# Kernel tuning notes

Hardware: AMD Instinct MI355X
Metric: run time of the kernel (lower is better)

Reference implementation:

```python
import jax, jax.numpy as jnp
import numpy as np


def setup_inputs() -> dict:
    key = jax.random.key(0)
    k1, k2, k3 = jax.random.split(key, 3)
    N, E, D_IN, D_OUT = 100000, 3200000, 256, 256
    x = jax.random.normal(k1, (N, D_IN), dtype=jnp.float32)
    W = jax.random.normal(k2, (D_OUT, D_IN), dtype=jnp.float32) * (1.0 / np.sqrt(D_IN))
    edge_index = jax.random.randint(k3, (2, E), 0, N, dtype=jnp.int32)
    return {"x": x, "W": W, "edge_index": edge_index}


def reference(x, W, edge_index):
    N = x.shape[0]
    # add self loops (static shape: E + N edges)
    loops = jnp.arange(N, dtype=edge_index.dtype)
    src = jnp.concatenate([edge_index[0], loops])  # [E+N]
    dst = jnp.concatenate([edge_index[1], loops])  # [E+N]
    # symmetric degree normalization: deg = bincount over source index
    deg = jax.ops.segment_sum(jnp.ones_like(src, dtype=x.dtype), src, num_segments=N)
    deg_rsqrt = jax.lax.rsqrt(deg)
    vals = deg_rsqrt[src] * deg_rsqrt[dst]  # [E+N]
    # dense projection then SpMM: out[i] = sum_e A[src_e=i] * h[dst_e]
    h = x @ W.T  # [N, D_OUT]
    msgs = vals[:, None] * h[dst]  # gather + scale
    out = jax.ops.segment_sum(msgs, src, num_segments=N)  # scatter-add
    return out
```

## Files before the change

kernel.cpp:

```cpp
#include <hip/hip_runtime.h>
#include <hip/hip_bf16.h>
#include <stdint.h>

#define D 256
#define NBUCK 391
#define BSHIFT 8
#define TILE 4096

typedef short short8 __attribute__((ext_vector_type(8)));
typedef float f32x4 __attribute__((ext_vector_type(4)));

__device__ __forceinline__ float bf2f(unsigned short u) {
  return __uint_as_float(((unsigned)u) << 16);
}
__device__ __forceinline__ unsigned short f2bf(float f) {
  unsigned u = __float_as_uint(f);
  unsigned r = u + 0x7FFFu + ((u >> 16) & 1u);
  return (unsigned short)(r >> 16);
}

__global__ void bucket_hist_kernel(const int* __restrict__ src, int* __restrict__ bcount, int E) {
  __shared__ int h[NBUCK];
  for (int i = threadIdx.x; i < NBUCK; i += 256) h[i] = 0;
  __syncthreads();
  int gid = blockIdx.x * 256 + threadIdx.x;
  for (int e = gid; e < E; e += 256 * 256) atomicAdd(&h[src[e] >> BSHIFT], 1);
  __syncthreads();
  for (int i = threadIdx.x; i < NBUCK; i += 256) {
    int c = h[i];
    if (c) atomicAdd(&bcount[i], c);
  }
}

__global__ void bucket_scan_kernel(const int* __restrict__ bcount, int* __restrict__ bbase,
                                   int* __restrict__ gcursor) {
  __shared__ int sc[2][512];
  int tid = threadIdx.x;
  sc[0][tid] = (tid < NBUCK) ? bcount[tid] : 0;
  __syncthreads();
  int d = 0;
  for (int off = 1; off < 512; off <<= 1) {
    int v = sc[d][tid];
    if (tid >= off) v += sc[d][tid - off];
    sc[d ^ 1][tid] = v;
    __syncthreads();
    d ^= 1;
  }
  if (tid < NBUCK) {
    int excl = (tid == 0) ? 0 : sc[d][tid - 1];
    bbase[tid] = excl;
    gcursor[tid] = excl;
  }
}

__launch_bounds__(256)
__global__ void binscatter_kernel(const int* __restrict__ src, const int* __restrict__ dst,
                                  int* __restrict__ gcursor, int* __restrict__ ebuf, int E) {
  __shared__ int hist[NBUCK];
  __shared__ int lstart[512];
  __shared__ int gbase[NBUCK];
  __shared__ int sc[2][512];
  __shared__ int stag[TILE];
  __shared__ unsigned short sbuck[TILE];

  int tid = threadIdx.x;
  int base = blockIdx.x * TILE;
  int tilecount = E - base;
  if (tilecount > TILE) tilecount = TILE;

  for (int i = tid; i < NBUCK; i += 256) hist[i] = 0;
  __syncthreads();

  int esrc[16], edst[16];
#pragma unroll
  for (int k = 0; k < 16; k++) {
    int e = base + k * 256 + tid;
    if (e < E) {
      esrc[k] = src[e];
      edst[k] = dst[e];
      atomicAdd(&hist[esrc[k] >> BSHIFT], 1);
    } else {
      esrc[k] = -1;
      edst[k] = 0;
    }
  }
  __syncthreads();

  for (int i = tid; i < 512; i += 256) sc[0][i] = (i < NBUCK) ? hist[i] : 0;
  __syncthreads();
  int d = 0;
  for (int off = 1; off < 512; off <<= 1) {
    for (int i = tid; i < 512; i += 256) {
      int v = sc[d][i];
      if (i >= off) v += sc[d][i - off];
      sc[d ^ 1][i] = v;
    }
    __syncthreads();
    d ^= 1;
  }
  for (int i = tid; i < 512; i += 256) lstart[i] = (i == 0) ? 0 : sc[d][i - 1];
  __syncthreads();

  for (int b = tid; b < NBUCK; b += 256) {
    int c = hist[b];
    if (c) gbase[b] = atomicAdd(&gcursor[b], c);
  }
  __syncthreads();

  for (int i = tid; i < NBUCK; i += 256) hist[i] = 0;
  __syncthreads();

#pragma unroll
  for (int k = 0; k < 16; k++) {
    if (esrc[k] >= 0) {
      int b = esrc[k] >> BSHIFT;
      int r = atomicAdd(&hist[b], 1);
      int pos = lstart[b] + r;
      stag[pos] = edst[k] | ((esrc[k] & 255) << 20);
      sbuck[pos] = (unsigned short)b;
    }
  }
  __syncthreads();

  for (int s = tid; s < tilecount; s += 256) {
    int b = sbuck[s];
    ebuf[gbase[b] + (s - lstart[b])] = stag[s];
  }
}

__launch_bounds__(256)
__global__ void bucketsort_kernel(const int* __restrict__ ebuf, const int* __restrict__ bbase,
                                  const int* __restrict__ bcount, int* __restrict__ csr,
                                  int* __restrict__ offsets, int* __restrict__ ecount,
                                  float* __restrict__ rnorm, int N) {
  __shared__ int ncnt[256];
  __shared__ int nstart[256];
  __shared__ int sc[2][256];
  int tid = threadIdx.x;
  int b = blockIdx.x;
  int base = bbase[b];
  int cnt = bcount[b];
  int node0 = b << BSHIFT;

  ncnt[tid] = 0;
  __syncthreads();
  for (int s = tid; s < cnt; s += 256) {
    int v = ebuf[base + s];
    atomicAdd(&ncnt[v >> 20], 1);
  }
  __syncthreads();

  int mycnt = ncnt[tid];
  sc[0][tid] = mycnt;
  __syncthreads();
  int d = 0;
  for (int off = 1; off < 256; off <<= 1) {
    int v = sc[d][tid];
    if (tid >= off) v += sc[d][tid - off];
    sc[d ^ 1][tid] = v;
    __syncthreads();
    d ^= 1;
  }
  nstart[tid] = (tid == 0) ? 0 : sc[d][tid - 1];
  __syncthreads();

  int node = node0 + tid;
  if (node < N) {
    offsets[node] = base + nstart[tid];
    ecount[node] = mycnt;
    rnorm[node] = rsqrtf((float)(mycnt + 1));
  }

  ncnt[tid] = 0;
  __syncthreads();
  for (int s = tid; s < cnt; s += 256) {
    int v = ebuf[base + s];
    int nl = v >> 20;
    int r = atomicAdd(&ncnt[nl], 1);
    csr[base + nstart[nl] + r] = v & 0xFFFFF;
  }
}

__global__ void convx_kernel(const float* __restrict__ x, unsigned short* __restrict__ xb,
                             int n, int npad) {
  int i4 = blockIdx.x * 256 + threadIdx.x;
  long long elem = (long long)i4 * 4;
  if (elem >= (long long)npad * D) return;
  int row = (int)(elem / D);
  ushort4 o;
  if (row < n) {
    const float4 v = *(const float4*)&x[elem];
    o.x = f2bf(v.x); o.y = f2bf(v.y); o.z = f2bf(v.z); o.w = f2bf(v.w);
  } else {
    o = make_ushort4(0, 0, 0, 0);
  }
  *(ushort4*)&xb[elem] = o;
}

__global__ void convw_kernel(const float* __restrict__ w, unsigned short* __restrict__ wb) {
  int i4 = blockIdx.x * 256 + threadIdx.x;
  int elem = i4 * 4;
  const float4 v = *(const float4*)&w[elem];
  ushort4 o;
  o.x = f2bf(v.x); o.y = f2bf(v.y); o.z = f2bf(v.z); o.w = f2bf(v.w);
  *(ushort4*)&wb[elem] = o;
}

__launch_bounds__(256)
__global__ void gemm_kernel(const unsigned short* __restrict__ A,
                            const unsigned short* __restrict__ B,
                            unsigned short* __restrict__ Hout,
                            const float* __restrict__ rnorm, int n) {
  __shared__ unsigned short sA[128 * 32];
  __shared__ unsigned short sB[128 * 32];
  int tid = threadIdx.x;
  int wave = tid >> 6, lane = tid & 63;
  int wm = wave >> 1, wn = wave & 1;
  int l16 = lane & 15, quad = lane >> 4;
  int arow0 = blockIdx.x * 128;
  int brow0 = blockIdx.y * 128;

  f32x4 acc[4][4];
  const f32x4 zero = {0.f, 0.f, 0.f, 0.f};
#pragma unroll
  for (int i = 0; i < 4; i++)
#pragma unroll
    for (int j = 0; j < 4; j++) acc[i][j] = zero;

  for (int k0 = 0; k0 < 256; k0 += 32) {
#pragma unroll
    for (int it = 0; it < 2; ++it) {
      int c = it * 256 + tid;
      int row = c >> 2, cc = (c & 3) * 8;
      *(int4*)&sA[c * 8] = *(const int4*)&A[(arow0 + row) * 256 + k0 + cc];
      *(int4*)&sB[c * 8] = *(const int4*)&B[(brow0 + row) * 256 + k0 + cc];
    }
    __syncthreads();
    short8 af[4], bfr[4];
#pragma unroll
    for (int i = 0; i < 4; i++)
      af[i] = *(const short8*)&sA[(wm * 64 + i * 16 + l16) * 32 + quad * 8];
#pragma unroll
    for (int j = 0; j < 4; j++)
      bfr[j] = *(const short8*)&sB[(wn * 64 + j * 16 + l16) * 32 + quad * 8];
#pragma unroll
    for (int i = 0; i < 4; i++)
#pragma unroll
      for (int j = 0; j < 4; j++)
        acc[i][j] = __builtin_amdgcn_mfma_f32_16x16x32_bf16(af[i], bfr[j], acc[i][j], 0, 0, 0);
    __syncthreads();
  }

#pragma unroll
  for (int i = 0; i < 4; i++) {
    int rowb = arow0 + wm * 64 + i * 16 + quad * 4;
#pragma unroll
    for (int r = 0; r < 4; r++) {
      int gr = rowb + r;
      float rn = (gr < n) ? rnorm[gr] : 0.f;
#pragma unroll
      for (int j = 0; j < 4; j++) {
        int col = brow0 + wn * 64 + j * 16 + l16;
        Hout[gr * 256 + col] = f2bf(acc[i][j][r] * rn);
      }
    }
  }
}

__launch_bounds__(256)
__global__ void gather_kernel(const unsigned short* __restrict__ hs,
                              const int* __restrict__ offsets,
                              const int* __restrict__ ecount,
                              const float* __restrict__ rnorm,
                              const int* __restrict__ csr,
                              float* __restrict__ out, int n, int colbase) {
  int wave = threadIdx.x >> 6, lane = threadIdx.x & 63;
  int node = blockIdx.x * 4 + wave;
  if (node >= n) return;
  int start = offsets[node], cnt = ecount[node];
  const unsigned short* hcol = hs + colbase + lane * 2;
  float a0 = 0.f, a1 = 0.f;
  for (int base = 0; base < cnt; base += 64) {
    int m = cnt - base;
    if (m > 64) m = 64;
    int idxv = 0;
    if (lane < m) idxv = csr[start + base + lane];
    int t = 0;
    for (; t + 8 <= m; t += 8) {
      int d0 = __shfl(idxv, t);
      int d1 = __shfl(idxv, t + 1);
      int d2 = __shfl(idxv, t + 2);
      int d3 = __shfl(idxv, t + 3);
      int d4 = __shfl(idxv, t + 4);
      int d5 = __shfl(idxv, t + 5);
      int d6 = __shfl(idxv, t + 6);
      int d7 = __shfl(idxv, t + 7);
      unsigned u0 = *(const unsigned*)&hcol[d0 * 256];
      unsigned u1 = *(const unsigned*)&hcol[d1 * 256];
      unsigned u2 = *(const unsigned*)&hcol[d2 * 256];
      unsigned u3 = *(const unsigned*)&hcol[d3 * 256];
      unsigned u4 = *(const unsigned*)&hcol[d4 * 256];
      unsigned u5 = *(const unsigned*)&hcol[d5 * 256];
      unsigned u6 = *(const unsigned*)&hcol[d6 * 256];
      unsigned u7 = *(const unsigned*)&hcol[d7 * 256];
      a0 += bf2f((unsigned short)u0) + bf2f((unsigned short)u1) +
            bf2f((unsigned short)u2) + bf2f((unsigned short)u3) +
            bf2f((unsigned short)u4) + bf2f((unsigned short)u5) +
            bf2f((unsigned short)u6) + bf2f((unsigned short)u7);
      a1 += bf2f((unsigned short)(u0 >> 16)) + bf2f((unsigned short)(u1 >> 16)) +
            bf2f((unsigned short)(u2 >> 16)) + bf2f((unsigned short)(u3 >> 16)) +
            bf2f((unsigned short)(u4 >> 16)) + bf2f((unsigned short)(u5 >> 16)) +
            bf2f((unsigned short)(u6 >> 16)) + bf2f((unsigned short)(u7 >> 16));
    }
    for (; t < m; ++t) {
      int dd = __shfl(idxv, t);
      unsigned u = *(const unsigned*)&hcol[dd * 256];
      a0 += bf2f((unsigned short)u);
      a1 += bf2f((unsigned short)(u >> 16));
    }
  }
  unsigned us = *(const unsigned*)&hcol[node * 256];
  float rn = rnorm[node];
  float2 o;
  o.x = rn * (a0 + bf2f((unsigned short)us));
  o.y = rn * (a1 + bf2f((unsigned short)(us >> 16)));
  *(float2*)&out[node * 256 + colbase + lane * 2] = o;
}

extern "C" void kernel_launch(void* const* d_in, const int* in_sizes, int n_in,
                              void* d_out, int out_size, void* d_ws, size_t ws_size,
                              hipStream_t stream) {
  const float* x = (const float*)d_in[0];
  const float* W = (const float*)d_in[1];
  const int* ei = (const int*)d_in[2];
  float* out = (float*)d_out;

  int N = in_sizes[0] / D;
  int E = in_sizes[2] / 2;
  int NPAD = (N + 127) & ~127;
  const int* src = ei;
  const int* dst = ei + E;

  char* p = (char*)d_ws;
  auto alloc = [&](size_t b) {
    char* r = p;
    p += (b + 255) & ~(size_t)255;
    return r;
  };
  unsigned short* xb = (unsigned short*)alloc((size_t)NPAD * D * 2);
  unsigned short* wb = (unsigned short*)alloc((size_t)D * D * 2);
  unsigned short* hb = (unsigned short*)alloc((size_t)NPAD * D * 2);
  int* csr = (int*)alloc((size_t)E * 4);
  int* offsets = (int*)alloc((size_t)N * 4);
  int* ecount = (int*)alloc((size_t)N * 4);
  float* rnorm = (float*)alloc((size_t)N * 4);
  int* bcount = (int*)alloc(NBUCK * 4);
  int* bbase = (int*)alloc(NBUCK * 4);
  int* gcursor = (int*)alloc(NBUCK * 4);
  int* ebuf = (int*)hb;

  hipMemsetAsync(bcount, 0, NBUCK * 4, stream);
  bucket_hist_kernel<<<256, 256, 0, stream>>>(src, bcount, E);
  bucket_scan_kernel<<<1, 512, 0, stream>>>(bcount, bbase, gcursor);
  binscatter_kernel<<<(E + TILE - 1) / TILE, 256, 0, stream>>>(src, dst, gcursor, ebuf, E);
  bucketsort_kernel<<<NBUCK, 256, 0, stream>>>(ebuf, bbase, bcount, csr, offsets, ecount, rnorm, N);
  convx_kernel<<<(NPAD * (D / 4) + 255) / 256, 256, 0, stream>>>(x, xb, N, NPAD);
  convw_kernel<<<(D * D / 4) / 256, 256, 0, stream>>>(W, wb);
  gemm_kernel<<<dim3(NPAD / 128, D / 128), 256, 0, stream>>>(xb, wb, hb, rnorm, N);
  gather_kernel<<<(N + 3) / 4, 256, 0, stream>>>(hb, offsets, ecount, rnorm, csr, out, N, 0);
  gather_kernel<<<(N + 3) / 4, 256, 0, stream>>>(hb, offsets, ecount, rnorm, csr, out, N, 128);
}
```

Baseline: 527.4 us.

## Store projected features in 16-column blocked layout and gather per column slice

The GEMM epilogue now writes H in a column-blocked layout: 16 slices of 16 bf16 columns, each contiguous over nodes. The gather is rewritten so each block interleaves 8 column-slice phases, and each wave processes 8 nodes. Within a wave, 8 lane groups each read 32-byte rows for different edges and are combined by a cross-lane reduction. Each pass touches a 3.2MB slice so the working set stays in cache, at the cost of more launches-per-node work, rereading CSR indices 16 times, and less coalesced 32-byte accesses.

```diff
diff --git a/kernel.cpp b/kernel.cpp
--- a/kernel.cpp
+++ b/kernel.cpp
@@ -9,6 +9,7 @@
 
 typedef short short8 __attribute__((ext_vector_type(8)));
 typedef float f32x4 __attribute__((ext_vector_type(4)));
+typedef float f32x2 __attribute__((ext_vector_type(2)));
 
 __device__ __forceinline__ float bf2f(unsigned short u) {
   return __uint_as_float(((unsigned)u) << 16);
@@ -210,7 +211,7 @@
 __global__ void gemm_kernel(const unsigned short* __restrict__ A,
                             const unsigned short* __restrict__ B,
                             unsigned short* __restrict__ Hout,
-                            const float* __restrict__ rnorm, int n) {
+                            const float* __restrict__ rnorm, int n, int npad) {
   __shared__ unsigned short sA[128 * 32];
   __shared__ unsigned short sB[128 * 32];
   int tid = threadIdx.x;
@@ -251,6 +252,7 @@
     __syncthreads();
   }
 
+  int cbbase = (brow0 >> 4) + wn * 4;
 #pragma unroll
   for (int i = 0; i < 4; i++) {
     int rowb = arow0 + wm * 64 + i * 16 + quad * 4;
@@ -260,71 +262,83 @@
       float rn = (gr < n) ? rnorm[gr] : 0.f;
 #pragma unroll
       for (int j = 0; j < 4; j++) {
-        int col = brow0 + wn * 64 + j * 16 + l16;
-        Hout[gr * 256 + col] = f2bf(acc[i][j][r] * rn);
+        Hout[((size_t)(cbbase + j) * npad + gr) * 16 + l16] = f2bf(acc[i][j][r] * rn);
       }
     }
   }
 }
 
 __launch_bounds__(256)
-__global__ void gather_kernel(const unsigned short* __restrict__ hs,
-                              const int* __restrict__ offsets,
-                              const int* __restrict__ ecount,
-                              const float* __restrict__ rnorm,
-                              const int* __restrict__ csr,
-                              float* __restrict__ out, int n, int colbase) {
-  int wave = threadIdx.x >> 6, lane = threadIdx.x & 63;
-  int node = blockIdx.x * 4 + wave;
-  if (node >= n) return;
-  int start = offsets[node], cnt = ecount[node];
-  const unsigned short* hcol = hs + colbase + lane * 2;
-  float a0 = 0.f, a1 = 0.f;
-  for (int base = 0; base < cnt; base += 64) {
-    int m = cnt - base;
-    if (m > 64) m = 64;
-    int idxv = 0;
-    if (lane < m) idxv = csr[start + base + lane];
-    int t = 0;
-    for (; t + 8 <= m; t += 8) {
-      int d0 = __shfl(idxv, t);
-      int d1 = __shfl(idxv, t + 1);
-      int d2 = __shfl(idxv, t + 2);
-      int d3 = __shfl(idxv, t + 3);
-      int d4 = __shfl(idxv, t + 4);
-      int d5 = __shfl(idxv, t + 5);
-      int d6 = __shfl(idxv, t + 6);
-      int d7 = __shfl(idxv, t + 7);
-      unsigned u0 = *(const unsigned*)&hcol[d0 * 256];
-      unsigned u1 = *(const unsigned*)&hcol[d1 * 256];
-      unsigned u2 = *(const unsigned*)&hcol[d2 * 256];
-      unsigned u3 = *(const unsigned*)&hcol[d3 * 256];
-      unsigned u4 = *(const unsigned*)&hcol[d4 * 256];
-      unsigned u5 = *(const unsigned*)&hcol[d5 * 256];
-      unsigned u6 = *(const unsigned*)&hcol[d6 * 256];
-      unsigned u7 = *(const unsigned*)&hcol[d7 * 256];
-      a0 += bf2f((unsigned short)u0) + bf2f((unsigned short)u1) +
-            bf2f((unsigned short)u2) + bf2f((unsigned short)u3) +
-            bf2f((unsigned short)u4) + bf2f((unsigned short)u5) +
-            bf2f((unsigned short)u6) + bf2f((unsigned short)u7);
-      a1 += bf2f((unsigned short)(u0 >> 16)) + bf2f((unsigned short)(u1 >> 16)) +
-            bf2f((unsigned short)(u2 >> 16)) + bf2f((unsigned short)(u3 >> 16)) +
-            bf2f((unsigned short)(u4 >> 16)) + bf2f((unsigned short)(u5 >> 16)) +
-            bf2f((unsigned short)(u6 >> 16)) + bf2f((unsigned short)(u7 >> 16));
-    }
-    for (; t < m; ++t) {
-      int dd = __shfl(idxv, t);
-      unsigned u = *(const unsigned*)&hcol[dd * 256];
-      a0 += bf2f((unsigned short)u);
-      a1 += bf2f((unsigned short)(u >> 16));
-    }
-  }
-  unsigned us = *(const unsigned*)&hcol[node * 256];
-  float rn = rnorm[node];
-  float2 o;
-  o.x = rn * (a0 + bf2f((unsigned short)us));
-  o.y = rn * (a1 + bf2f((unsigned short)(us >> 16)));
-  *(float2*)&out[node * 256 + colbase + lane * 2] = o;
+__global__ void gather_phase_kernel(const unsigned short* __restrict__ hsb,
+                                    const int* __restrict__ offsets,
+                                    const int* __restrict__ ecount,
+                                    const float* __restrict__ rnorm,
+                                    const int* __restrict__ csr,
+                                    float* __restrict__ out,
+                                    int n, int npad, int pbase) {
+  const int wave = threadIdx.x >> 6;
+  const int lane = threadIdx.x & 63;
+  const int phase = blockIdx.x & 7;
+  const int grp = blockIdx.x >> 3;
+  const int cb = pbase + phase;
+  const int g = lane >> 3;
+  const int c = lane & 7;
+  const unsigned short* slice = hsb + (size_t)cb * npad * 16;
+
+  int node0 = grp * 32 + wave * 8;
+#pragma unroll 1
+  for (int ni = 0; ni < 8; ++ni) {
+    int node = node0 + ni;
+    if (node >= n) break;
+    int start = __builtin_nontemporal_load(&offsets[node]);
+    int cnt = __builtin_nontemporal_load(&ecount[node]);
+    float a0 = 0.f, a1 = 0.f;
+    for (int base = 0; base < cnt; base += 64) {
+      int m = cnt - base;
+      if (m > 64) m = 64;
+      int idxv = 0;
+      if (lane < m) idxv = __builtin_nontemporal_load(&csr[start + base + lane]);
+      int t = 0;
+      for (; t + 32 <= m; t += 32) {
+        int d0 = __shfl(idxv, t + g);
+        int d1 = __shfl(idxv, t + 8 + g);
+        int d2 = __shfl(idxv, t + 16 + g);
+        int d3 = __shfl(idxv, t + 24 + g);
+        unsigned u0 = *(const unsigned*)&slice[d0 * 16 + c * 2];
+        unsigned u1 = *(const unsigned*)&slice[d1 * 16 + c * 2];
+        unsigned u2 = *(const unsigned*)&slice[d2 * 16 + c * 2];
+        unsigned u3 = *(const unsigned*)&slice[d3 * 16 + c * 2];
+        a0 += bf2f((unsigned short)u0) + bf2f((unsigned short)u1) +
+              bf2f((unsigned short)u2) + bf2f((unsigned short)u3);
+        a1 += bf2f((unsigned short)(u0 >> 16)) + bf2f((unsigned short)(u1 >> 16)) +
+              bf2f((unsigned short)(u2 >> 16)) + bf2f((unsigned short)(u3 >> 16));
+      }
+      for (; t + 8 <= m; t += 8) {
+        int d0 = __shfl(idxv, t + g);
+        unsigned u0 = *(const unsigned*)&slice[d0 * 16 + c * 2];
+        a0 += bf2f((unsigned short)u0);
+        a1 += bf2f((unsigned short)(u0 >> 16));
+      }
+      if (t < m) {
+        int d0 = __shfl(idxv, t + g);
+        unsigned u0 = 0;
+        if (g < m - t) u0 = *(const unsigned*)&slice[d0 * 16 + c * 2];
+        a0 += bf2f((unsigned short)u0);
+        a1 += bf2f((unsigned short)(u0 >> 16));
+      }
+    }
+    a0 += __shfl_xor(a0, 8);  a1 += __shfl_xor(a1, 8);
+    a0 += __shfl_xor(a0, 16); a1 += __shfl_xor(a1, 16);
+    a0 += __shfl_xor(a0, 32); a1 += __shfl_xor(a1, 32);
+    if (g == 0) {
+      unsigned us = *(const unsigned*)&slice[node * 16 + c * 2];
+      float rn = rnorm[node];
+      f32x2 o;
+      o.x = rn * (a0 + bf2f((unsigned short)us));
+      o.y = rn * (a1 + bf2f((unsigned short)(us >> 16)));
+      __builtin_nontemporal_store(o, (f32x2*)&out[(size_t)node * 256 + cb * 16 + c * 2]);
+    }
+  }
 }
 
 extern "C" void kernel_launch(void* const* d_in, const int* in_sizes, int n_in,
@@ -366,7 +380,9 @@
   bucketsort_kernel<<<NBUCK, 256, 0, stream>>>(ebuf, bbase, bcount, csr, offsets, ecount, rnorm, N);
   convx_kernel<<<(NPAD * (D / 4) + 255) / 256, 256, 0, stream>>>(x, xb, N, NPAD);
   convw_kernel<<<(D * D / 4) / 256, 256, 0, stream>>>(W, wb);
-  gemm_kernel<<<dim3(NPAD / 128, D / 128), 256, 0, stream>>>(xb, wb, hb, rnorm, N);
-  gather_kernel<<<(N + 3) / 4, 256, 0, stream>>>(hb, offsets, ecount, rnorm, csr, out, N, 0);
-  gather_kernel<<<(N + 3) / 4, 256, 0, stream>>>(hb, offsets, ecount, rnorm, csr, out, N, 128);
-}
+  gemm_kernel<<<dim3(NPAD / 128, D / 128), 256, 0, stream>>>(xb, wb, hb, rnorm, N, NPAD);
+
+  int ngrp = (N + 31) / 32;
+  gather_phase_kernel<<<8 * ngrp, 256, 0, stream>>>(hb, offsets, ecount, rnorm, csr, out, N, NPAD, 0);
+  gather_phase_kernel<<<8 * ngrp, 256, 0, stream>>>(hb, offsets, ecount, rnorm, csr, out, N, NPAD, 8);
+}
```

Result: slower. 1.032 ms (+95.7%).

## Fuse fp32-to-bf16 conversion of x into GEMM and merge gather launches

Applied to the files above, without the earlier changes.

Drops the separate convx kernel: the GEMM now loads fp32 x directly and converts it to bf16 while staging tiles into shared memory. This removes one full write and re-read of the bf16 copy of x. The two per-column-half gather launches become one launch that interleaves column halves by block index, and the per-node offset and count arrays are packed into one int2 so a single 8-byte load fetches both. The GEMM now reads twice the bytes of the A operand per tile, and each A tile is read by both column-block workgroups.

```diff
diff --git a/kernel.cpp b/kernel.cpp
--- a/kernel.cpp
+++ b/kernel.cpp
@@ -131,8 +131,7 @@
 __launch_bounds__(256)
 __global__ void bucketsort_kernel(const int* __restrict__ ebuf, const int* __restrict__ bbase,
                                   const int* __restrict__ bcount, int* __restrict__ csr,
-                                  int* __restrict__ offsets, int* __restrict__ ecount,
-                                  float* __restrict__ rnorm, int N) {
+                                  int2* __restrict__ meta, float* __restrict__ rnorm, int N) {
   __shared__ int ncnt[256];
   __shared__ int nstart[256];
   __shared__ int sc[2][256];
@@ -166,8 +165,7 @@
 
   int node = node0 + tid;
   if (node < N) {
-    offsets[node] = base + nstart[tid];
-    ecount[node] = mycnt;
+    meta[node] = make_int2(base + nstart[tid], mycnt);
     rnorm[node] = rsqrtf((float)(mycnt + 1));
   }
 
@@ -179,22 +177,6 @@
     int r = atomicAdd(&ncnt[nl], 1);
     csr[base + nstart[nl] + r] = v & 0xFFFFF;
   }
-}
-
-__global__ void convx_kernel(const float* __restrict__ x, unsigned short* __restrict__ xb,
-                             int n, int npad) {
-  int i4 = blockIdx.x * 256 + threadIdx.x;
-  long long elem = (long long)i4 * 4;
-  if (elem >= (long long)npad * D) return;
-  int row = (int)(elem / D);
-  ushort4 o;
-  if (row < n) {
-    const float4 v = *(const float4*)&x[elem];
-    o.x = f2bf(v.x); o.y = f2bf(v.y); o.z = f2bf(v.z); o.w = f2bf(v.w);
-  } else {
-    o = make_ushort4(0, 0, 0, 0);
-  }
-  *(ushort4*)&xb[elem] = o;
 }
 
 __global__ void convw_kernel(const float* __restrict__ w, unsigned short* __restrict__ wb) {
@@ -207,7 +189,7 @@
 }
 
 __launch_bounds__(256)
-__global__ void gemm_kernel(const unsigned short* __restrict__ A,
+__global__ void gemm_kernel(const float* __restrict__ X,
                             const unsigned short* __restrict__ B,
                             unsigned short* __restrict__ Hout,
                             const float* __restrict__ rnorm, int n) {
@@ -232,7 +214,16 @@
     for (int it = 0; it < 2; ++it) {
       int c = it * 256 + tid;
       int row = c >> 2, cc = (c & 3) * 8;
-      *(int4*)&sA[c * 8] = *(const int4*)&A[(arow0 + row) * 256 + k0 + cc];
+      int grow = arow0 + row;
+      ushort4 lo = make_ushort4(0, 0, 0, 0), hi = make_ushort4(0, 0, 0, 0);
+      if (grow < n) {
+        const float4 v0 = *(const float4*)&X[(size_t)grow * 256 + k0 + cc];
+        const float4 v1 = *(const float4*)&X[(size_t)grow * 256 + k0 + cc + 4];
+        lo.x = f2bf(v0.x); lo.y = f2bf(v0.y); lo.z = f2bf(v0.z); lo.w = f2bf(v0.w);
+        hi.x = f2bf(v1.x); hi.y = f2bf(v1.y); hi.z = f2bf(v1.z); hi.w = f2bf(v1.w);
+      }
+      *(ushort4*)&sA[c * 8] = lo;
+      *(ushort4*)&sA[c * 8 + 4] = hi;
       *(int4*)&sB[c * 8] = *(const int4*)&B[(brow0 + row) * 256 + k0 + cc];
     }
     __syncthreads();
@@ -261,7 +252,7 @@
 #pragma unroll
       for (int j = 0; j < 4; j++) {
         int col = brow0 + wn * 64 + j * 16 + l16;
-        Hout[gr * 256 + col] = f2bf(acc[i][j][r] * rn);
+        Hout[(size_t)gr * 256 + col] = f2bf(acc[i][j][r] * rn);
       }
     }
   }
@@ -269,15 +260,16 @@
 
 __launch_bounds__(256)
 __global__ void gather_kernel(const unsigned short* __restrict__ hs,
-                              const int* __restrict__ offsets,
-                              const int* __restrict__ ecount,
+                              const int2* __restrict__ meta,
                               const float* __restrict__ rnorm,
                               const int* __restrict__ csr,
-                              float* __restrict__ out, int n, int colbase) {
+                              float* __restrict__ out, int n) {
   int wave = threadIdx.x >> 6, lane = threadIdx.x & 63;
-  int node = blockIdx.x * 4 + wave;
+  int colbase = (blockIdx.x & 1) * 128;
+  int node = (blockIdx.x >> 1) * 4 + wave;
   if (node >= n) return;
-  int start = offsets[node], cnt = ecount[node];
+  long long mm = *(const long long*)&meta[node];
+  int start = (int)mm, cnt = (int)(mm >> 32);
   const unsigned short* hcol = hs + colbase + lane * 2;
   float a0 = 0.f, a1 = 0.f;
   for (int base = 0; base < cnt; base += 64) {
@@ -324,7 +316,7 @@
   float2 o;
   o.x = rn * (a0 + bf2f((unsigned short)us));
   o.y = rn * (a1 + bf2f((unsigned short)(us >> 16)));
-  *(float2*)&out[node * 256 + colbase + lane * 2] = o;
+  *(float2*)&out[(size_t)node * 256 + colbase + lane * 2] = o;
 }
 
 extern "C" void kernel_launch(void* const* d_in, const int* in_sizes, int n_in,
@@ -347,12 +339,10 @@
     p += (b + 255) & ~(size_t)255;
     return r;
   };
-  unsigned short* xb = (unsigned short*)alloc((size_t)NPAD * D * 2);
   unsigned short* wb = (unsigned short*)alloc((size_t)D * D * 2);
   unsigned short* hb = (unsigned short*)alloc((size_t)NPAD * D * 2);
-  int* csr = (int*)alloc((size_t)E * 4);
-  int* offsets = (int*)alloc((size_t)N * 4);
-  int* ecount = (int*)alloc((size_t)N * 4);
+  int* csr = (int*)alloc((size_t)(E + 64) * 4);
+  int2* meta = (int2*)alloc((size_t)N * 8);
   float* rnorm = (float*)alloc((size_t)N * 4);
   int* bcount = (int*)alloc(NBUCK * 4);
   int* bbase = (int*)alloc(NBUCK * 4);
@@ -363,10 +353,8 @@
   bucket_hist_kernel<<<256, 256, 0, stream>>>(src, bcount, E);
   bucket_scan_kernel<<<1, 512, 0, stream>>>(bcount, bbase, gcursor);
   binscatter_kernel<<<(E + TILE - 1) / TILE, 256, 0, stream>>>(src, dst, gcursor, ebuf, E);
-  bucketsort_kernel<<<NBUCK, 256, 0, stream>>>(ebuf, bbase, bcount, csr, offsets, ecount, rnorm, N);
-  convx_kernel<<<(NPAD * (D / 4) + 255) / 256, 256, 0, stream>>>(x, xb, N, NPAD);
+  bucketsort_kernel<<<NBUCK, 256, 0, stream>>>(ebuf, bbase, bcount, csr, meta, rnorm, N);
   convw_kernel<<<(D * D / 4) / 256, 256, 0, stream>>>(W, wb);
-  gemm_kernel<<<dim3(NPAD / 128, D / 128), 256, 0, stream>>>(xb, wb, hb, rnorm, N);
-  gather_kernel<<<(N + 3) / 4, 256, 0, stream>>>(hb, offsets, ecount, rnorm, csr, out, N, 0);
-  gather_kernel<<<(N + 3) / 4, 256, 0, stream>>>(hb, offsets, ecount, rnorm, csr, out, N, 128);
-}
+  gemm_kernel<<<dim3(NPAD / 128, D / 128), 256, 0, stream>>>(x, wb, hb, rnorm, N);
+  gather_kernel<<<2 * ((N + 3) / 4), 256, 0, stream>>>(hb, meta, rnorm, csr, out, N);
+}
```

New measurement: 520.8 us. About the same (-1.2%).
